# Performance work log

Measured on AMD Instinct MI355X. Metric: run time of the kernel, lower is better.

The kernel has to match this reference:

```python
import jax, jax.numpy as jnp
import numpy as np

N = 100000   # nodes
E = 1600000  # edges (avg degree 16)
H = 128      # hidden
S = 10000    # subgraphs
G = 64       # graphs


def setup_inputs() -> dict:
    key = jax.random.key(0)
    ks = jax.random.split(key, 8)
    def w(k, shape, fan_in):
        return jax.random.normal(k, shape, dtype=jnp.float32) * (1.0 / np.sqrt(fan_in))
    return {
        "x": jnp.ones((N, 1), dtype=jnp.float32),
        "edge_index": jax.random.randint(ks[0], (2, E), 0, N, dtype=jnp.int64),
        "node_to_subgraph": jnp.sort(jax.random.randint(ks[1], (N,), 0, S, dtype=jnp.int64)),
        "subgraph_to_graph": jnp.sort(jax.random.randint(ks[2], (S,), 0, G, dtype=jnp.int64)),
        "conv1_W1": w(ks[3], (1, H), 1),
        "conv1_b1": jnp.zeros((H,), jnp.float32),
        "conv1_W2": w(ks[4], (H, H), H),
        "conv1_b2": jnp.zeros((H,), jnp.float32),
        "convs_W1": w(ks[5], (2, H, H), H),
        "convs_b1": jnp.zeros((2, H), jnp.float32),
        "convs_W2": w(ks[6], (2, H, H), H),
        "convs_b2": jnp.zeros((2, H), jnp.float32),
    }


def _gin_layer(x, src, dst, W1, b1, W2, b2):
    # GINConv, train_eps=False, eps=0: nn((1+0)*x + sum_{j in N(i)} x_j)
    agg = jax.ops.segment_sum(x[src], dst, num_segments=x.shape[0])
    h = jax.nn.relu((x + agg) @ W1 + b1)
    return jax.nn.relu(h @ W2 + b2)


def reference(x, edge_index, node_to_subgraph, subgraph_to_graph,
              conv1_W1, conv1_b1, conv1_W2, conv1_b2,
              convs_W1, convs_b1, convs_W2, convs_b2):
    src, dst = edge_index[0], edge_index[1]
    h = _gin_layer(x, src, dst, conv1_W1, conv1_b1, conv1_W2, conv1_b2)
    for i in range(convs_W1.shape[0]):  # num_layers - 1 = 2 structurally distinct layers
        h = _gin_layer(h, src, dst, convs_W1[i], convs_b1[i], convs_W2[i], convs_b2[i])
    # global_add_pool over node_to_subgraph, then subgraph_to_graph
    h = jax.ops.segment_sum(h, node_to_subgraph, num_segments=S)
    h = jax.ops.segment_sum(h, subgraph_to_graph, num_segments=G)
    return h  # [G, H]
```

## Files before the change

kernel.cpp:

```cpp
#include <hip/hip_runtime.h>

typedef unsigned int u32;
typedef unsigned short u16;
typedef __attribute__((ext_vector_type(8))) short bf16x8;
typedef __attribute__((ext_vector_type(4))) float f32x4;

#define CAP 2560
#define CHUNK 8192
#define GMT 2

__device__ __forceinline__ float bfl(u32 v){ return __uint_as_float(v << 16); }
__device__ __forceinline__ float bfh(u32 v){ return __uint_as_float(v & 0xffff0000u); }
__device__ __forceinline__ u16 f2bf(float f){
    u32 u = __float_as_uint(f);
    u += 0x7fffu + ((u >> 16) & 1u);
    return (u16)(u >> 16);
}
__device__ __forceinline__ u32 pack2(float a, float b){
    u32 ua = __float_as_uint(a); ua += 0x7fffu + ((ua >> 16) & 1u);
    u32 ub = __float_as_uint(b); ub += 0x7fffu + ((ub >> 16) & 1u);
    return (ua >> 16) | (ub & 0xffff0000u);
}


__global__ __launch_bounds__(256) void bucket_count(const int* __restrict__ dst,
                                                    const int* __restrict__ src,
                                                    int* __restrict__ gcur,
                                                    u32* __restrict__ slots,
                                                    int NBk, int E){
    __shared__ int cnt[800];
    int t = threadIdx.x;
    int e0 = blockIdx.x * CHUNK;
    for (int i = t; i < NBk; i += 256) cnt[i] = 0;
    __syncthreads();
    #pragma unroll
    for (int k = 0; k < CHUNK / 256; k++){
        int e = e0 + t + k * 256;
        if (e < E) atomicAdd(&cnt[dst[e] >> 7], 1);
    }
    __syncthreads();
    for (int i = t; i < NBk; i += 256){
        int c = cnt[i];
        cnt[i] = c ? atomicAdd(&gcur[i], c) : 0;
    }
    __syncthreads();
    #pragma unroll
    for (int k = 0; k < CHUNK / 256; k++){
        int e = e0 + t + k * 256;
        if (e < E){
            int d = dst[e];
            int b = d >> 7;
            int pos = atomicAdd(&cnt[b], 1);
            if (pos < CAP) slots[b * CAP + pos] = ((u32)(d & 127) << 17) | (u32)src[e];
        }
    }
}

__global__ __launch_bounds__(256) void bucket_csr(const int* __restrict__ gcur,
                                                  u32* __restrict__ csr,
                                                  int* __restrict__ starts,
                                                  int* __restrict__ ends, int N){
    __shared__ u32 ebuf[CAP];
    __shared__ int cnt[128], excl[128], cur[128];
    int b = blockIdx.x, t = threadIdx.x;
    int base = b * CAP;
    int sz = gcur[b]; if (sz > CAP) sz = CAP;
    if (t < 128) cnt[t] = 0;
    __syncthreads();
    for (int i = t; i < sz; i += 256){
        u32 p = csr[base + i];
        ebuf[i] = p;
        atomicAdd(&cnt[p >> 17], 1);
    }
    __syncthreads();
    if (t < 64){
        int c0 = cnt[2 * t], c1 = cnt[2 * t + 1];
        int tot = c0 + c1;
        int incl = tot;
        #pragma unroll
        for (int o = 1; o < 64; o <<= 1){
            int v = __shfl_up(incl, o);
            if (t >= o) incl += v;
        }
        int ex = incl - tot;
        excl[2 * t] = ex;
        excl[2 * t + 1] = ex + c0;
    }
    __syncthreads();
    if (t < 128){
        int node = b * 128 + t;
        if (node < N){
            int st = base + excl[t];
            starts[node] = st;
            ends[node] = st + cnt[t];
        }
        cur[t] = excl[t];
    }
    __syncthreads();
    for (int i = t; i < sz; i += 256){
        u32 p = ebuf[i];
        int dl = p >> 17;
        int r = atomicAdd(&cur[dl], 1);
        csr[base + r] = p & 0x1FFFFu;
    }
}


__global__ __launch_bounds__(256) void sumx_gmap(const float* __restrict__ x,
                                                 const u32* __restrict__ csr,
                                                 const int* __restrict__ starts,
                                                 const int* __restrict__ ends,
                                                 const int* __restrict__ n2s,
                                                 const int* __restrict__ s2g,
                                                 float* __restrict__ sval,
                                                 int* __restrict__ gmap, int N){
    int gtid = blockIdx.x * 256 + threadIdx.x;
    int node = gtid >> 2;
    int ln = threadIdx.x & 3;
    if (node >= N) return;
    int b0 = starts[node], b1 = ends[node];
    float a = 0.f;
    for (int j = b0 + ln; j < b1; j += 4) a += x[csr[j]];
    a += __shfl_xor(a, 1);
    a += __shfl_xor(a, 2);
    if (ln == 0){
        sval[node] = x[node] + a;
        gmap[node] = s2g[n2s[node]];
    }
}


struct W5 { const float* p[5]; };

__global__ void pack_k(W5 w5, u16* __restrict__ wp){
    int m = blockIdx.x;
    const float* W = w5.p[m];
    u16* dstp = wp + m * 16384;
    int t = threadIdx.x;
    #pragma unroll
    for (int it = 0; it < 8; it++){
        int task = t + 256 * it;
        int n = task & 127, c = task >> 7;
        u16 tmp[8];
        #pragma unroll
        for (int j = 0; j < 8; j++) tmp[j] = f2bf(W[(c * 8 + j) * 128 + n]);
        uint4 val;
        val.x = (u32)tmp[0] | ((u32)tmp[1] << 16);
        val.y = (u32)tmp[2] | ((u32)tmp[3] << 16);
        val.z = (u32)tmp[4] | ((u32)tmp[5] << 16);
        val.w = (u32)tmp[6] | ((u32)tmp[7] << 16);
        *(uint4*)(dstp + n * 128 + ((c ^ ((n >> 3) & 15)) << 3)) = val;
    }
}


__global__ __launch_bounds__(256) void gemm1_fused(const float* __restrict__ sval,
                                                   const float* __restrict__ W1,
                                                   const float* __restrict__ b1,
                                                   const u16* __restrict__ Wp,
                                                   const float* __restrict__ bias,
                                                   u16* __restrict__ Out, int nrows){
    __shared__ uint4 ldsbuf[2048];
    __shared__ float w1s[128], b1s[128];
    u16* lds = (u16*)ldsbuf;
    int t = threadIdx.x;
    const uint4* wsrc = (const uint4*)Wp;
    #pragma unroll
    for (int j = 0; j < 8; j++) ldsbuf[t + 256 * j] = wsrc[t + 256 * j];
    if (t < 128){ w1s[t] = W1[t]; b1s[t] = b1[t]; }
    __syncthreads();

    int wave = t >> 6, lane = t & 63;
    int m = lane & 15, q = lane >> 4;
    int r0 = blockIdx.x * (64 * GMT) + wave * (16 * GMT);

    float sv[GMT];
    #pragma unroll
    for (int mt = 0; mt < GMT; mt++){
        int row = r0 + mt * 16 + m;
        if (row >= nrows) row = nrows - 1;
        sv[mt] = sval[row];
    }

    f32x4 acc[GMT][8];
    #pragma unroll
    for (int a = 0; a < GMT; a++)
        #pragma unroll
        for (int b = 0; b < 8; b++){ f32x4 z = {0.f, 0.f, 0.f, 0.f}; acc[a][b] = z; }

    #pragma unroll
    for (int kt = 0; kt < 4; kt++){
        int c = kt * 4 + q;
        int k0 = kt * 32 + q * 8;
        float wk[8], bk[8];
        #pragma unroll
        for (int j = 0; j < 8; j++){ wk[j] = w1s[k0 + j]; bk[j] = b1s[k0 + j]; }
        bf16x8 bfrag[8];
        #pragma unroll
        for (int nt = 0; nt < 8; nt++){
            int n = m * 8 + nt;
            bfrag[nt] = *(const bf16x8*)(lds + n * 128 + ((c ^ m) << 3));
        }
        #pragma unroll
        for (int mt = 0; mt < GMT; mt++){
            bf16x8 afrag;
            #pragma unroll
            for (int j = 0; j < 8; j++){
                float v = sv[mt] * wk[j] + bk[j];
                v = v > 0.f ? v : 0.f;
                afrag[j] = (short)f2bf(v);
            }
            #pragma unroll
            for (int nt = 0; nt < 8; nt++)
                acc[mt][nt] = __builtin_amdgcn_mfma_f32_16x16x32_bf16(afrag, bfrag[nt], acc[mt][nt], 0, 0, 0);
        }
    }

    float4 bb0 = *(const float4*)(bias + m * 8);
    float4 bb1 = *(const float4*)(bias + m * 8 + 4);
    float bb[8] = {bb0.x, bb0.y, bb0.z, bb0.w, bb1.x, bb1.y, bb1.z, bb1.w};
    #pragma unroll
    for (int mt = 0; mt < GMT; mt++){
        #pragma unroll
        for (int r = 0; r < 4; r++){
            int row = r0 + mt * 16 + q * 4 + r;
            if (row < nrows){
                float v[8];
                #pragma unroll
                for (int j = 0; j < 8; j++){
                    float vv = acc[mt][j][r] + bb[j];
                    v[j] = vv > 0.f ? vv : 0.f;
                }
                uint4 o;
                o.x = pack2(v[0], v[1]);
                o.y = pack2(v[2], v[3]);
                o.z = pack2(v[4], v[5]);
                o.w = pack2(v[6], v[7]);
                *(uint4*)(Out + row * 128 + m * 8) = o;
            }
        }
    }
}


__global__ __launch_bounds__(256) void gemm_relu(const u16* A, const u16* __restrict__ Wp,
                                                 const float* __restrict__ bias,
                                                 u16* Out, int nrows){
    __shared__ uint4 ldsbuf[2048];
    u16* lds = (u16*)ldsbuf;
    int t = threadIdx.x;
    const uint4* wsrc = (const uint4*)Wp;
    #pragma unroll
    for (int j = 0; j < 8; j++) ldsbuf[t + 256 * j] = wsrc[t + 256 * j];
    __syncthreads();

    int wave = t >> 6, lane = t & 63;
    int m = lane & 15, q = lane >> 4;
    int r0 = blockIdx.x * (64 * GMT) + wave * (16 * GMT);

    f32x4 acc[GMT][8];
    #pragma unroll
    for (int a = 0; a < GMT; a++)
        #pragma unroll
        for (int b = 0; b < 8; b++){ f32x4 z = {0.f, 0.f, 0.f, 0.f}; acc[a][b] = z; }

    #pragma unroll
    for (int kt = 0; kt < 4; kt++){
        int c = kt * 4 + q;
        bf16x8 bfrag[8];
        #pragma unroll
        for (int nt = 0; nt < 8; nt++){
            int n = m * 8 + nt;
            bfrag[nt] = *(const bf16x8*)(lds + n * 128 + ((c ^ m) << 3));
        }
        #pragma unroll
        for (int mt = 0; mt < GMT; mt++){
            int row = r0 + mt * 16 + m;
            if (row >= nrows) row = nrows - 1;
            bf16x8 afrag = *(const bf16x8*)(A + row * 128 + kt * 32 + q * 8);
            #pragma unroll
            for (int nt = 0; nt < 8; nt++)
                acc[mt][nt] = __builtin_amdgcn_mfma_f32_16x16x32_bf16(afrag, bfrag[nt], acc[mt][nt], 0, 0, 0);
        }
    }

    float4 bb0 = *(const float4*)(bias + m * 8);
    float4 bb1 = *(const float4*)(bias + m * 8 + 4);
    float bb[8] = {bb0.x, bb0.y, bb0.z, bb0.w, bb1.x, bb1.y, bb1.z, bb1.w};
    #pragma unroll
    for (int mt = 0; mt < GMT; mt++){
        #pragma unroll
        for (int r = 0; r < 4; r++){
            int row = r0 + mt * 16 + q * 4 + r;
            if (row < nrows){
                float v[8];
                #pragma unroll
                for (int j = 0; j < 8; j++){
                    float vv = acc[mt][j][r] + bb[j];
                    v[j] = vv > 0.f ? vv : 0.f;
                }
                uint4 o;
                o.x = pack2(v[0], v[1]);
                o.y = pack2(v[2], v[3]);
                o.z = pack2(v[4], v[5]);
                o.w = pack2(v[6], v[7]);
                *(uint4*)(Out + row * 128 + m * 8) = o;
            }
        }
    }
}


__device__ __forceinline__ void acc8(float* a, uint4 u){
    a[0] += bfl(u.x); a[1] += bfh(u.x);
    a[2] += bfl(u.y); a[3] += bfh(u.y);
    a[4] += bfl(u.z); a[5] += bfh(u.z);
    a[6] += bfl(u.w); a[7] += bfh(u.w);
}

__global__ __launch_bounds__(256) void agg_k(const uint4* __restrict__ Hin, uint4* __restrict__ Hout,
                                             const int* __restrict__ starts, const int* __restrict__ ends,
                                             const u32* __restrict__ csr, int N){
    int gtid = blockIdx.x * 256 + threadIdx.x;
    int node = gtid >> 4;
    int c = threadIdx.x & 15;
    if (node >= N) return;

    uint4 v = Hin[node * 16 + c];
    float a[8];
    a[0] = bfl(v.x); a[1] = bfh(v.x);
    a[2] = bfl(v.y); a[3] = bfh(v.y);
    a[4] = bfl(v.z); a[5] = bfh(v.z);
    a[6] = bfl(v.w); a[7] = bfh(v.w);

    int b0 = starts[node], b1 = ends[node];
    int j = b0;
    for (; j + 4 <= b1; j += 4){
        int s0 = csr[j], s1 = csr[j + 1], s2 = csr[j + 2], s3 = csr[j + 3];
        uint4 u0 = Hin[s0 * 16 + c];
        uint4 u1 = Hin[s1 * 16 + c];
        uint4 u2 = Hin[s2 * 16 + c];
        uint4 u3 = Hin[s3 * 16 + c];
        acc8(a, u0); acc8(a, u1); acc8(a, u2); acc8(a, u3);
    }
    for (; j < b1; j++){
        int s = csr[j];
        uint4 u = Hin[s * 16 + c];
        acc8(a, u);
    }

    uint4 o;
    o.x = pack2(a[0], a[1]);
    o.y = pack2(a[2], a[3]);
    o.z = pack2(a[4], a[5]);
    o.w = pack2(a[6], a[7]);
    Hout[node * 16 + c] = o;
}


__global__ __launch_bounds__(256) void pool2_k(const u32* __restrict__ H,
                                               const int* __restrict__ gmap,
                                               float* __restrict__ out, int N){
    int c = threadIdx.x & 63;
    int seg = blockIdx.x * 4 + (threadIdx.x >> 6);
    int start = seg * 64;
    if (start >= N) return;
    int end = start + 64; if (end > N) end = N;
    int g = gmap[start];
    float a0 = 0.f, a1 = 0.f;
    for (int n = start; n < end; n++){
        int gn = gmap[n];
        if (gn != g){
            unsafeAtomicAdd(&out[g * 128 + 2 * c], a0);
            unsafeAtomicAdd(&out[g * 128 + 2 * c + 1], a1);
            a0 = 0.f; a1 = 0.f; g = gn;
        }
        u32 u = H[n * 64 + c];
        a0 += bfl(u);
        a1 += bfh(u);
    }
    unsafeAtomicAdd(&out[g * 128 + 2 * c], a0);
    unsafeAtomicAdd(&out[g * 128 + 2 * c + 1], a1);
}

extern "C" void kernel_launch(void* const* d_in, const int* in_sizes, int n_in,
                              void* d_out, int out_size, void* d_ws, size_t ws_size,
                              hipStream_t stream){
    const float* x    = (const float*)d_in[0];
    const int*   ei   = (const int*)d_in[1];
    const int*   n2s  = (const int*)d_in[2];
    const int*   s2g  = (const int*)d_in[3];
    const float* c1W1 = (const float*)d_in[4];
    const float* c1b1 = (const float*)d_in[5];
    const float* c1W2 = (const float*)d_in[6];
    const float* c1b2 = (const float*)d_in[7];
    const float* cW1  = (const float*)d_in[8];
    const float* cb1  = (const float*)d_in[9];
    const float* cW2  = (const float*)d_in[10];
    const float* cb2  = (const float*)d_in[11];
    float* out = (float*)d_out;

    int N = in_sizes[0];
    int E = in_sizes[1] / 2;
    const int* src = ei;
    const int* dst = ei + E;
    int NBk = (N + 127) / 128;

    char* w = (char*)d_ws;
    size_t off = 0;
    auto al = [&](size_t b){ size_t r = off; off += (b + 255) & ~(size_t)255; return r; };
    int*   gcur   = (int*)(w + al((size_t)NBk * 4));
    int*   starts = (int*)(w + al((size_t)N * 4));
    int*   ends   = (int*)(w + al((size_t)N * 4));
    float* sval   = (float*)(w + al((size_t)N * 4));
    int*   gmap   = (int*)(w + al((size_t)N * 4));
    u32*   csr    = (u32*)(w + al((size_t)NBk * CAP * 4));
    u16*   wp     = (u16*)(w + al((size_t)5 * 16384 * 2));
    u16*   P      = (u16*)(w + al((size_t)N * 128 * 2));
    u16*   Q      = (u16*)(w + al((size_t)N * 128 * 2));

    hipMemsetAsync(gcur, 0, (size_t)NBk * 4, stream);
    hipMemsetAsync(out, 0, (size_t)out_size * 4, stream);

    W5 w5;
    w5.p[0] = c1W2;
    w5.p[1] = cW1;
    w5.p[2] = cW2;
    w5.p[3] = cW1 + 16384;
    w5.p[4] = cW2 + 16384;
    pack_k<<<5, 256, 0, stream>>>(w5, wp);

    bucket_count<<<(E + CHUNK - 1) / CHUNK, 256, 0, stream>>>(dst, src, gcur, csr, NBk, E);
    bucket_csr<<<NBk, 256, 0, stream>>>(gcur, csr, starts, ends, N);
    sumx_gmap<<<(N * 4 + 255) / 256, 256, 0, stream>>>(x, csr, starts, ends, n2s, s2g, sval, gmap, N);

    int gG = (N + 64 * GMT - 1) / (64 * GMT);
    int gA = (N * 16 + 255) / 256;
    gemm1_fused<<<gG, 256, 0, stream>>>(sval, c1W1, c1b1, wp + 0 * 16384, c1b2, P, N);
    agg_k<<<gA, 256, 0, stream>>>((const uint4*)P, (uint4*)Q, starts, ends, csr, N);
    gemm_relu<<<gG, 256, 0, stream>>>(Q, wp + 1 * 16384, cb1, Q, N);
    gemm_relu<<<gG, 256, 0, stream>>>(Q, wp + 2 * 16384, cb2, Q, N);
    agg_k<<<gA, 256, 0, stream>>>((const uint4*)Q, (uint4*)P, starts, ends, csr, N);
    gemm_relu<<<gG, 256, 0, stream>>>(P, wp + 3 * 16384, cb1 + 128, P, N);
    gemm_relu<<<gG, 256, 0, stream>>>(P, wp + 4 * 16384, cb2 + 128, P, N);
    pool2_k<<<(N + 255) / 256, 256, 0, stream>>>((const u32*)P, gmap, out, N);
}
```

Before: 360.1 us.

## Fuse back-to-back GEMM pairs, fold neighbor-sum into CSR build, drop memsets

Merges the two consecutive 128x128 GEMM+ReLU kernels of each GIN MLP into one kernel. The intermediate activation tile stays in swizzled LDS instead of round-tripping through global memory. Folds the layer-1 scalar neighbor sum and graph-map computation into the bucket CSR build using shared-memory float atomics, and replaces the two memsets with extra blocks in the weight-pack kernel. The fused GEMM doubles LDS use per block, which may lower occupancy, and float atomic ordering makes the first-layer sum order nondeterministic.

```diff
diff --git a/kernel.cpp b/kernel.cpp
--- a/kernel.cpp
+++ b/kernel.cpp
@@ -56,21 +56,29 @@
     }
 }
 
+
 __global__ __launch_bounds__(256) void bucket_csr(const int* __restrict__ gcur,
                                                   u32* __restrict__ csr,
                                                   int* __restrict__ starts,
-                                                  int* __restrict__ ends, int N){
+                                                  int* __restrict__ ends,
+                                                  const float* __restrict__ x,
+                                                  const int* __restrict__ n2s,
+                                                  const int* __restrict__ s2g,
+                                                  float* __restrict__ sval,
+                                                  int* __restrict__ gmap, int N){
     __shared__ u32 ebuf[CAP];
     __shared__ int cnt[128], excl[128], cur[128];
+    __shared__ float sacc[128];
     int b = blockIdx.x, t = threadIdx.x;
     int base = b * CAP;
     int sz = gcur[b]; if (sz > CAP) sz = CAP;
-    if (t < 128) cnt[t] = 0;
+    if (t < 128){ cnt[t] = 0; sacc[t] = 0.f; }
     __syncthreads();
     for (int i = t; i < sz; i += 256){
         u32 p = csr[base + i];
         ebuf[i] = p;
         atomicAdd(&cnt[p >> 17], 1);
+        atomicAdd(&sacc[p >> 17], x[p & 0x1FFFFu]);
     }
     __syncthreads();
     if (t < 64){
@@ -93,6 +101,8 @@
             int st = base + excl[t];
             starts[node] = st;
             ends[node] = st + cnt[t];
+            sval[node] = x[node] + sacc[t];
+            gmap[node] = s2g[n2s[node]];
         }
         cur[t] = excl[t];
     }
@@ -106,37 +116,23 @@
 }
 
 
-__global__ __launch_bounds__(256) void sumx_gmap(const float* __restrict__ x,
-                                                 const u32* __restrict__ csr,
-                                                 const int* __restrict__ starts,
-                                                 const int* __restrict__ ends,
-                                                 const int* __restrict__ n2s,
-                                                 const int* __restrict__ s2g,
-                                                 float* __restrict__ sval,
-                                                 int* __restrict__ gmap, int N){
-    int gtid = blockIdx.x * 256 + threadIdx.x;
-    int node = gtid >> 2;
-    int ln = threadIdx.x & 3;
-    if (node >= N) return;
-    int b0 = starts[node], b1 = ends[node];
-    float a = 0.f;
-    for (int j = b0 + ln; j < b1; j += 4) a += x[csr[j]];
-    a += __shfl_xor(a, 1);
-    a += __shfl_xor(a, 2);
-    if (ln == 0){
-        sval[node] = x[node] + a;
-        gmap[node] = s2g[n2s[node]];
-    }
-}
-
-
 struct W5 { const float* p[5]; };
 
-__global__ void pack_k(W5 w5, u16* __restrict__ wp){
+__global__ void pack_k(W5 w5, u16* __restrict__ wp,
+                       int* __restrict__ gcur, int ngcur,
+                       float* __restrict__ outz, int nout){
     int m = blockIdx.x;
+    int t = threadIdx.x;
+    if (m == 5){
+        for (int i = t; i < ngcur; i += 256) gcur[i] = 0;
+        return;
+    }
+    if (m == 6){
+        for (int i = t; i < nout; i += 256) outz[i] = 0.f;
+        return;
+    }
     const float* W = w5.p[m];
     u16* dstp = wp + m * 16384;
-    int t = threadIdx.x;
     #pragma unroll
     for (int it = 0; it < 8; it++){
         int task = t + 256 * it;
@@ -243,20 +239,28 @@
 }
 
 
-__global__ __launch_bounds__(256) void gemm_relu(const u16* A, const u16* __restrict__ Wp,
-                                                 const float* __restrict__ bias,
-                                                 u16* Out, int nrows){
-    __shared__ uint4 ldsbuf[2048];
-    u16* lds = (u16*)ldsbuf;
+__global__ __launch_bounds__(256) void gemm2_fused(const u16* A,
+                                                   const u16* __restrict__ Wp1,
+                                                   const u16* __restrict__ Wp2,
+                                                   const float* __restrict__ bias1,
+                                                   const float* __restrict__ bias2,
+                                                   u16* Out, int nrows){
+    __shared__ uint4 buf1[2048];
+    __shared__ uint4 buf2[2048];
+    u16* lds1 = (u16*)buf1;
+    u16* lds2 = (u16*)buf2;
     int t = threadIdx.x;
-    const uint4* wsrc = (const uint4*)Wp;
-    #pragma unroll
-    for (int j = 0; j < 8; j++) ldsbuf[t + 256 * j] = wsrc[t + 256 * j];
+    #pragma unroll
+    for (int j = 0; j < 8; j++){
+        buf1[t + 256 * j] = ((const uint4*)Wp1)[t + 256 * j];
+        buf2[t + 256 * j] = ((const uint4*)Wp2)[t + 256 * j];
+    }
     __syncthreads();
 
     int wave = t >> 6, lane = t & 63;
     int m = lane & 15, q = lane >> 4;
-    int r0 = blockIdx.x * (64 * GMT) + wave * (16 * GMT);
+    int rl0 = wave * (16 * GMT);
+    int r0 = blockIdx.x * (64 * GMT) + rl0;
 
     f32x4 acc[GMT][8];
     #pragma unroll
@@ -271,7 +275,7 @@
         #pragma unroll
         for (int nt = 0; nt < 8; nt++){
             int n = m * 8 + nt;
-            bfrag[nt] = *(const bf16x8*)(lds + n * 128 + ((c ^ m) << 3));
+            bfrag[nt] = *(const bf16x8*)(lds1 + n * 128 + ((c ^ m) << 3));
         }
         #pragma unroll
         for (int mt = 0; mt < GMT; mt++){
@@ -283,9 +287,60 @@
                 acc[mt][nt] = __builtin_amdgcn_mfma_f32_16x16x32_bf16(afrag, bfrag[nt], acc[mt][nt], 0, 0, 0);
         }
     }
-
-    float4 bb0 = *(const float4*)(bias + m * 8);
-    float4 bb1 = *(const float4*)(bias + m * 8 + 4);
+    __syncthreads();
+
+    {
+        float4 bb0 = *(const float4*)(bias1 + m * 8);
+        float4 bb1 = *(const float4*)(bias1 + m * 8 + 4);
+        float bb[8] = {bb0.x, bb0.y, bb0.z, bb0.w, bb1.x, bb1.y, bb1.z, bb1.w};
+        #pragma unroll
+        for (int mt = 0; mt < GMT; mt++){
+            #pragma unroll
+            for (int r = 0; r < 4; r++){
+                int rl = rl0 + mt * 16 + q * 4 + r;
+                float v[8];
+                #pragma unroll
+                for (int j = 0; j < 8; j++){
+                    float vv = acc[mt][j][r] + bb[j];
+                    v[j] = vv > 0.f ? vv : 0.f;
+                }
+                uint4 o;
+                o.x = pack2(v[0], v[1]);
+                o.y = pack2(v[2], v[3]);
+                o.z = pack2(v[4], v[5]);
+                o.w = pack2(v[6], v[7]);
+                *(uint4*)(lds1 + rl * 128 + ((m ^ (rl & 15)) << 3)) = o;
+            }
+        }
+    }
+    __syncthreads();
+
+    #pragma unroll
+    for (int a = 0; a < GMT; a++)
+        #pragma unroll
+        for (int b = 0; b < 8; b++){ f32x4 z = {0.f, 0.f, 0.f, 0.f}; acc[a][b] = z; }
+
+    #pragma unroll
+    for (int kt = 0; kt < 4; kt++){
+        int c = kt * 4 + q;
+        bf16x8 bfrag[8];
+        #pragma unroll
+        for (int nt = 0; nt < 8; nt++){
+            int n = m * 8 + nt;
+            bfrag[nt] = *(const bf16x8*)(lds2 + n * 128 + ((c ^ m) << 3));
+        }
+        #pragma unroll
+        for (int mt = 0; mt < GMT; mt++){
+            int rl = rl0 + mt * 16 + m;
+            bf16x8 afrag = *(const bf16x8*)(lds1 + rl * 128 + (((kt * 4 + q) ^ (rl & 15)) << 3));
+            #pragma unroll
+            for (int nt = 0; nt < 8; nt++)
+                acc[mt][nt] = __builtin_amdgcn_mfma_f32_16x16x32_bf16(afrag, bfrag[nt], acc[mt][nt], 0, 0, 0);
+        }
+    }
+
+    float4 bb0 = *(const float4*)(bias2 + m * 8);
+    float4 bb1 = *(const float4*)(bias2 + m * 8 + 4);
     float bb[8] = {bb0.x, bb0.y, bb0.z, bb0.w, bb1.x, bb1.y, bb1.z, bb1.w};
     #pragma unroll
     for (int mt = 0; mt < GMT; mt++){
@@ -419,29 +474,23 @@
     u16*   P      = (u16*)(w + al((size_t)N * 128 * 2));
     u16*   Q      = (u16*)(w + al((size_t)N * 128 * 2));
 
-    hipMemsetAsync(gcur, 0, (size_t)NBk * 4, stream);
-    hipMemsetAsync(out, 0, (size_t)out_size * 4, stream);
-
     W5 w5;
     w5.p[0] = c1W2;
     w5.p[1] = cW1;
     w5.p[2] = cW2;
     w5.p[3] = cW1 + 16384;
     w5.p[4] = cW2 + 16384;
-    pack_k<<<5, 256, 0, stream>>>(w5, wp);
+    pack_k<<<7, 256, 0, stream>>>(w5, wp, gcur, NBk, out, out_size);
 
     bucket_count<<<(E + CHUNK - 1) / CHUNK, 256, 0, stream>>>(dst, src, gcur, csr, NBk, E);
-    bucket_csr<<<NBk, 256, 0, stream>>>(gcur, csr, starts, ends, N);
-    sumx_gmap<<<(N * 4 + 255) / 256, 256, 0, stream>>>(x, csr, starts, ends, n2s, s2g, sval, gmap, N);
+    bucket_csr<<<NBk, 256, 0, stream>>>(gcur, csr, starts, ends, x, n2s, s2g, sval, gmap, N);
 
     int gG = (N + 64 * GMT - 1) / (64 * GMT);
     int gA = (N * 16 + 255) / 256;
     gemm1_fused<<<gG, 256, 0, stream>>>(sval, c1W1, c1b1, wp + 0 * 16384, c1b2, P, N);
     agg_k<<<gA, 256, 0, stream>>>((const uint4*)P, (uint4*)Q, starts, ends, csr, N);
-    gemm_relu<<<gG, 256, 0, stream>>>(Q, wp + 1 * 16384, cb1, Q, N);
-    gemm_relu<<<gG, 256, 0, stream>>>(Q, wp + 2 * 16384, cb2, Q, N);
+    gemm2_fused<<<gG, 256, 0, stream>>>(Q, wp + 1 * 16384, wp + 2 * 16384, cb1, cb2, Q, N);
     agg_k<<<gA, 256, 0, stream>>>((const uint4*)Q, (uint4*)P, starts, ends, csr, N);
-    gemm_relu<<<gG, 256, 0, stream>>>(P, wp + 3 * 16384, cb1 + 128, P, N);
-    gemm_relu<<<gG, 256, 0, stream>>>(P, wp + 4 * 16384, cb2 + 128, P, N);
+    gemm2_fused<<<gG, 256, 0, stream>>>(P, wp + 3 * 16384, wp + 4 * 16384, cb1 + 128, cb2 + 128, P, N);
     pool2_k<<<(N + 255) / 256, 256, 0, stream>>>((const u32*)P, gmap, out, N);
 }
```

Result: faster. 336.5 us (-6.6%).
